# Optimization experiments

Measured on AMD Instinct MI355X. Metric: run time of the kernel, lower is better.

Reference implementation:

```python
import jax, jax.numpy as jnp
import numpy as np

B, N = 128, 196
ENC, DEC, ATT = 2048, 512, 512

def setup_inputs() -> dict:
    key = jax.random.key(0)
    ks = jax.random.split(key, 8)
    s_enc = 1.0 / np.sqrt(ENC)
    s_dec = 1.0 / np.sqrt(DEC)
    s_att = 1.0 / np.sqrt(ATT)
    return {
        "encoder_out": jax.random.normal(ks[0], (B, N, ENC), jnp.float32),
        "decoder_hidden": jax.random.normal(ks[1], (B, DEC), jnp.float32),
        "W_enc": jax.random.uniform(ks[2], (ENC, ATT), jnp.float32, -s_enc, s_enc),
        "b_enc": jax.random.uniform(ks[3], (ATT,), jnp.float32, -s_enc, s_enc),
        "W_dec": jax.random.uniform(ks[4], (DEC, ATT), jnp.float32, -s_dec, s_dec),
        "b_dec": jax.random.uniform(ks[5], (ATT,), jnp.float32, -s_dec, s_dec),
        "W_full": jax.random.uniform(ks[6], (ATT,), jnp.float32, -s_att, s_att),
        "b_full": jax.random.uniform(ks[7], (), jnp.float32, -s_att, s_att),
    }

def reference(encoder_out, decoder_hidden, W_enc, b_enc, W_dec, b_dec, W_full, b_full):
    # att1: [B, N, ATT]; att2: [B, 1, ATT]
    att1 = jnp.einsum('bne,ea->bna', encoder_out, W_enc) + b_enc
    att2 = decoder_hidden @ W_dec + b_dec
    combined = jax.nn.relu(att1 + att2[:, None, :])
    e = jnp.einsum('bna,a->bn', combined, W_full) + b_full  # [B, N]
    alpha = jax.nn.softmax(e, axis=1)
    attention_weighted_encoding = jnp.einsum('bne,bn->be', encoder_out, alpha)
    return attention_weighted_encoding, alpha
```

## Files before the change

### kernel.cpp

```cpp
#include <hip/hip_runtime.h>
#include <hip/hip_bf16.h>

#define BB   128
#define NN   196
#define MM   (BB*NN)
#define ENC  2048
#define ATT  512
#define DEC  512
#define BK   32
#define KSTEPS (ENC/BK)

using f32x4 = __attribute__((ext_vector_type(4))) float;
using s16x8 = __attribute__((ext_vector_type(8))) short;

__device__ __forceinline__ short f2bf(float f) {
    union { __hip_bfloat16 h; short s; } u;
    u.h = __float2bfloat16(f);
    return u.s;
}

__global__ void transpose_convert_kernel(const float* __restrict__ W,
                                         unsigned short* __restrict__ Wt) {
    __shared__ float tile[32][33];
    const int a0 = blockIdx.x * 32;
    const int k0 = blockIdx.y * 32;
    const int tx = threadIdx.x & 31, ty = threadIdx.x >> 5;
    #pragma unroll
    for (int i = 0; i < 32; i += 8)
        tile[ty + i][tx] = W[(size_t)(k0 + ty + i) * ATT + a0 + tx];
    __syncthreads();
    #pragma unroll
    for (int i = 0; i < 32; i += 8) {
        union { __hip_bfloat16 h; unsigned short u; } v;
        v.h = __float2bfloat16(tile[tx][ty + i]);
        Wt[(size_t)(a0 + ty + i) * ENC + k0 + tx] = v.u;
    }
}

__global__ void att2_kernel(const float* __restrict__ dec,
                            const float* __restrict__ Wd,
                            const float* __restrict__ bd,
                            const float* __restrict__ benc,
                            float* __restrict__ att2) {
    const int b  = blockIdx.x;
    const int c0 = blockIdx.y * 64;
    const int t  = threadIdx.x;
    const int cl = t & 63, kg = t >> 6;
    __shared__ float sdec[DEC];
    __shared__ float red[4][64];
    sdec[t]       = dec[b * DEC + t];
    sdec[t + 256] = dec[b * DEC + t + 256];
    __syncthreads();
    float acc = 0.f;
    const float* wp = Wd + c0 + cl;
    #pragma unroll 8
    for (int k = kg * 128; k < kg * 128 + 128; ++k)
        acc += sdec[k] * wp[(size_t)k * ATT];
    red[kg][cl] = acc;
    __syncthreads();
    if (t < 64) {
        float s = red[0][t] + red[1][t] + red[2][t] + red[3][t];
        att2[b * ATT + c0 + t] = s + bd[c0 + t] + benc[c0 + t];
    }
}

__global__ __launch_bounds__(256, 3)
void gemm_e_kernel(const float* __restrict__ enc,
                   const unsigned short* __restrict__ Wt,
                   const float* __restrict__ att2,
                   const float* __restrict__ Wf,
                   float* __restrict__ e_part) {
    __shared__ unsigned short sA[2][64 * 40];
    __shared__ unsigned short sB[2][256 * 32];
    __shared__ float e_sm[64];

    const int t    = threadIdx.x;
    const int lane = t & 63;
    const int w    = t >> 6;
    const int aBlk  = blockIdx.x;
    const int mBase = blockIdx.y * 64;
    const int aBase = aBlk * 256;
    const int r = lane & 15, q = lane >> 4;

    const int arow = t >> 2;
    const int akc  = (t & 3) * 8;
    const float* gA = enc + (size_t)(mBase + arow) * ENC + akc;
    const int wAoff = arow * 40 + akc;

    const unsigned short* gB[4];
    #pragma unroll
    for (int i = 0; i < 4; ++i) {
        int s = i * 256 + t;
        int brow = s >> 2;
        int ck = (s & 3) ^ ((brow >> 1) & 3);
        gB[i] = Wt + (size_t)(aBase + brow) * ENC + ck * 8;
    }

    int offA[4];
    #pragma unroll
    for (int mi = 0; mi < 4; ++mi)
        offA[mi] = (mi * 16 + r) * 40 + q * 8;
    int offB[4];
    #pragma unroll
    for (int ni = 0; ni < 4; ++ni) {
        int col = w * 64 + ni * 16 + r;
        offB[ni] = col * 32 + (q ^ ((col >> 1) & 3)) * 8;
    }

    f32x4 acc[4][4] = {};

    auto issueB = [&](int ks, int buf) {
        #pragma unroll
        for (int i = 0; i < 4; ++i)
            __builtin_amdgcn_global_load_lds(
                (const __attribute__((address_space(1))) void*)(gB[i] + (size_t)ks * BK),
                (__attribute__((address_space(3))) void*)(&sB[buf][0] + (i * 256 + w * 64) * 8),
                16, 0, 0);
    };
    auto storeA = [&](int buf, f32x4 x0, f32x4 x1) {
        s16x8 v;
        #pragma unroll
        for (int j = 0; j < 4; ++j) { v[j] = f2bf(x0[j]); v[4 + j] = f2bf(x1[j]); }
        *(s16x8*)(&sA[buf][0] + wAoff) = v;
    };
    auto compute = [&](int buf) {
        s16x8 af[4], bf[4];
        #pragma unroll
        for (int mi = 0; mi < 4; ++mi)
            af[mi] = *(const s16x8*)(&sA[buf][0] + offA[mi]);
        #pragma unroll
        for (int ni = 0; ni < 4; ++ni)
            bf[ni] = *(const s16x8*)(&sB[buf][0] + offB[ni]);
        #pragma unroll
        for (int mi = 0; mi < 4; ++mi)
            #pragma unroll
            for (int ni = 0; ni < 4; ++ni)
                acc[mi][ni] = __builtin_amdgcn_mfma_f32_16x16x32_bf16(
                    af[mi], bf[ni], acc[mi][ni], 0, 0, 0);
    };

    f32x4 a0, a1;
    {
        const float* p = gA;
        a0 = *(const f32x4*)p; a1 = *(const f32x4*)(p + 4);
    }
    issueB(0, 0);
    storeA(0, a0, a1);
    __syncthreads();

    #pragma unroll 1
    for (int ks = 1; ks < KSTEPS; ++ks) {
        const float* p = gA + (size_t)ks * BK;
        a0 = *(const f32x4*)p; a1 = *(const f32x4*)(p + 4);
        issueB(ks, ks & 1);
        compute((ks - 1) & 1);
        storeA(ks & 1, a0, a1);
        __syncthreads();
    }
    compute((KSTEPS - 1) & 1);

    if (t < 64) e_sm[t] = 0.f;
    __syncthreads();

    float wfv[4];
    #pragma unroll
    for (int ni = 0; ni < 4; ++ni)
        wfv[ni] = Wf[aBase + w * 64 + ni * 16 + r];

    #pragma unroll
    for (int mi = 0; mi < 4; ++mi) {
        #pragma unroll
        for (int reg = 0; reg < 4; ++reg) {
            int lrow = mi * 16 + q * 4 + reg;
            int gm = mBase + lrow;
            int b = gm / NN;
            const float* a2 = att2 + b * ATT + aBase + w * 64;
            float rs = 0.f;
            #pragma unroll
            for (int ni = 0; ni < 4; ++ni) {
                float v = acc[mi][ni][reg] + a2[ni * 16 + r];
                rs += fmaxf(v, 0.f) * wfv[ni];
            }
            atomicAdd(&e_sm[lrow], rs);
        }
    }
    __syncthreads();
    if (t < 64)
        e_part[(size_t)aBlk * MM + mBase + t] = e_sm[t];
}

__global__ void softmax_kernel(const float* __restrict__ e_part,
                               const float* __restrict__ b_full,
                               float* __restrict__ out,
                               float* __restrict__ alpha_ws) {
    const int b = blockIdx.x;
    const int t = threadIdx.x;
    __shared__ float sm[256];

    float v = -3.0e38f;
    if (t < NN) {
        int gm = b * NN + t;
        v = e_part[gm] + e_part[MM + gm] + b_full[0];
    }
    sm[t] = v;
    __syncthreads();
    for (int s = 128; s > 0; s >>= 1) {
        if (t < s) sm[t] = fmaxf(sm[t], sm[t + s]);
        __syncthreads();
    }
    float mx = sm[0];
    __syncthreads();
    float ex = (t < NN) ? __expf(v - mx) : 0.f;
    sm[t] = ex;
    __syncthreads();
    for (int s = 128; s > 0; s >>= 1) {
        if (t < s) sm[t] += sm[t + s];
        __syncthreads();
    }
    float inv = 1.0f / sm[0];
    if (t < NN) {
        float a = ex * inv;
        out[BB * ENC + b * NN + t] = a;
        alpha_ws[b * NN + t] = a;
    }
}

__global__ __launch_bounds__(64)
void awe_kernel(const float* __restrict__ enc,
                const float* __restrict__ alpha_ws,
                float* __restrict__ out) {
    const int b = blockIdx.x, chunk = blockIdx.y;
    const int l = threadIdx.x;
    __shared__ float al[NN];
    for (int n = l; n < NN; n += 64) al[n] = alpha_ws[b * NN + n];
    __syncthreads();

    const float* ep = enc + (size_t)b * NN * ENC + chunk * 256 + l * 4;
    f32x4 acc0 = {}, acc1 = {}, acc2 = {}, acc3 = {};
    #pragma unroll 2
    for (int n = 0; n < NN; n += 4) {
        f32x4 v0 = *(const f32x4*)(ep + (size_t)(n + 0) * ENC);
        f32x4 v1 = *(const f32x4*)(ep + (size_t)(n + 1) * ENC);
        f32x4 v2 = *(const f32x4*)(ep + (size_t)(n + 2) * ENC);
        f32x4 v3 = *(const f32x4*)(ep + (size_t)(n + 3) * ENC);
        acc0 += v0 * al[n];
        acc1 += v1 * al[n + 1];
        acc2 += v2 * al[n + 2];
        acc3 += v3 * al[n + 3];
    }
    f32x4 s = (acc0 + acc1) + (acc2 + acc3);
    *(f32x4*)(out + (size_t)b * ENC + chunk * 256 + l * 4) = s;
}

extern "C" void kernel_launch(void* const* d_in, const int* in_sizes, int n_in,
                              void* d_out, int out_size, void* d_ws, size_t ws_size,
                              hipStream_t stream) {
    const float* enc    = (const float*)d_in[0];
    const float* dec    = (const float*)d_in[1];
    const float* W_enc  = (const float*)d_in[2];
    const float* b_enc  = (const float*)d_in[3];
    const float* W_dec  = (const float*)d_in[4];
    const float* b_dec  = (const float*)d_in[5];
    const float* W_full = (const float*)d_in[6];
    const float* b_full = (const float*)d_in[7];
    float* out = (float*)d_out;

    char* ws = (char*)d_ws;
    unsigned short* Wt = (unsigned short*)ws;
    float* att2     = (float*)(ws + (size_t)ENC * ATT * 2);
    float* e_part   = (float*)(ws + (size_t)ENC * ATT * 2 + BB * ATT * 4);
    float* alpha_ws = (float*)(ws + (size_t)ENC * ATT * 2 + BB * ATT * 4
                               + (size_t)2 * MM * 4);

    transpose_convert_kernel<<<dim3(ATT / 32, ENC / 32), 256, 0, stream>>>(W_enc, Wt);
    att2_kernel<<<dim3(BB, 8), 256, 0, stream>>>(dec, W_dec, b_dec, b_enc, att2);
    gemm_e_kernel<<<dim3(2, MM / 64), 256, 0, stream>>>(enc, Wt, att2, W_full, e_part);
    softmax_kernel<<<BB, 256, 0, stream>>>(e_part, b_full, out, alpha_ws);
    awe_kernel<<<dim3(BB, 8), 64, 0, stream>>>(enc, alpha_ws, out);
}
```

Before: 472.9 us.

## Narrow GEMM tile to 128 columns, stream fp32 A via LDS, single-buffer

The GEMM kernel now uses 64x128 tiles instead of 64x256, and four column blocks write partial scores that the softmax sums. Encoder rows are copied as fp32 straight into swizzled LDS with direct global-to-LDS loads and converted to bf16 at fragment-read time, replacing the register-staged conversion. Double buffering is dropped for a single buffer with two barriers per step, and occupancy is raised to 5 waves. This halves the row reuse of A, so the fp32 encoder is read four times instead of twice. The e reduction now uses shuffles before the LDS atomic, and the awe kernel uses 256-thread blocks.

```diff
diff --git a/kernel.cpp b/kernel.cpp
--- a/kernel.cpp
+++ b/kernel.cpp
@@ -64,14 +64,14 @@
     }
 }
 
-__global__ __launch_bounds__(256, 3)
+__global__ __launch_bounds__(256, 5)
 void gemm_e_kernel(const float* __restrict__ enc,
                    const unsigned short* __restrict__ Wt,
                    const float* __restrict__ att2,
                    const float* __restrict__ Wf,
                    float* __restrict__ e_part) {
-    __shared__ unsigned short sA[2][64 * 40];
-    __shared__ unsigned short sB[2][256 * 32];
+    __shared__ float sA[64 * 32];
+    __shared__ unsigned short sB[128 * 32];
     __shared__ float e_sm[64];
 
     const int t    = threadIdx.x;
@@ -79,93 +79,88 @@
     const int w    = t >> 6;
     const int aBlk  = blockIdx.x;
     const int mBase = blockIdx.y * 64;
-    const int aBase = aBlk * 256;
+    const int aBase = aBlk * 128;
     const int r = lane & 15, q = lane >> 4;
 
-    const int arow = t >> 2;
-    const int akc  = (t & 3) * 8;
-    const float* gA = enc + (size_t)(mBase + arow) * ENC + akc;
-    const int wAoff = arow * 40 + akc;
-
-    const unsigned short* gB[4];
-    #pragma unroll
-    for (int i = 0; i < 4; ++i) {
+    const float* gA[2];
+    #pragma unroll
+    for (int i = 0; i < 2; ++i) {
         int s = i * 256 + t;
-        int brow = s >> 2;
-        int ck = (s & 3) ^ ((brow >> 1) & 3);
-        gB[i] = Wt + (size_t)(aBase + brow) * ENC + ck * 8;
-    }
-
-    int offA[4];
-    #pragma unroll
-    for (int mi = 0; mi < 4; ++mi)
-        offA[mi] = (mi * 16 + r) * 40 + q * 8;
-    int offB[4];
-    #pragma unroll
-    for (int ni = 0; ni < 4; ++ni) {
-        int col = w * 64 + ni * 16 + r;
-        offB[ni] = col * 32 + (q ^ ((col >> 1) & 3)) * 8;
-    }
-
-    f32x4 acc[4][4] = {};
-
-    auto issueB = [&](int ks, int buf) {
-        #pragma unroll
-        for (int i = 0; i < 4; ++i)
+        int row = s >> 3, ck = s & 7;
+        int g = ck ^ (row & 7);
+        gA[i] = enc + (size_t)(mBase + row) * ENC + g * 4;
+    }
+    const unsigned short* gB[2];
+    #pragma unroll
+    for (int i = 0; i < 2; ++i) {
+        int s = i * 256 + t;
+        int row = s >> 2, ck = s & 3;
+        int g = ck ^ ((row & 3) ^ ((row >> 2) & 3));
+        gB[i] = Wt + (size_t)(aBase + row) * ENC + g * 8;
+    }
+
+    int offA[4][2];
+    #pragma unroll
+    for (int mi = 0; mi < 4; ++mi) {
+        int row = mi * 16 + r;
+        offA[mi][0] = row * 128 + ((2 * q)     ^ (row & 7)) * 16;
+        offA[mi][1] = row * 128 + ((2 * q + 1) ^ (row & 7)) * 16;
+    }
+    int offB[2];
+    #pragma unroll
+    for (int ni = 0; ni < 2; ++ni) {
+        int col = w * 32 + ni * 16 + r;
+        offB[ni] = col * 64 + (q ^ ((col & 3) ^ ((col >> 2) & 3))) * 16;
+    }
+
+    f32x4 acc[4][2] = {};
+
+    #pragma unroll 1
+    for (int ks = 0; ks < KSTEPS; ++ks) {
+        #pragma unroll
+        for (int i = 0; i < 2; ++i)
+            __builtin_amdgcn_global_load_lds(
+                (const __attribute__((address_space(1))) void*)(gA[i] + (size_t)ks * BK),
+                (__attribute__((address_space(3))) void*)((char*)sA + (i * 256 + w * 64) * 16),
+                16, 0, 0);
+        #pragma unroll
+        for (int i = 0; i < 2; ++i)
             __builtin_amdgcn_global_load_lds(
                 (const __attribute__((address_space(1))) void*)(gB[i] + (size_t)ks * BK),
-                (__attribute__((address_space(3))) void*)(&sB[buf][0] + (i * 256 + w * 64) * 8),
+                (__attribute__((address_space(3))) void*)((char*)sB + (i * 256 + w * 64) * 16),
                 16, 0, 0);
-    };
-    auto storeA = [&](int buf, f32x4 x0, f32x4 x1) {
-        s16x8 v;
-        #pragma unroll
-        for (int j = 0; j < 4; ++j) { v[j] = f2bf(x0[j]); v[4 + j] = f2bf(x1[j]); }
-        *(s16x8*)(&sA[buf][0] + wAoff) = v;
-    };
-    auto compute = [&](int buf) {
-        s16x8 af[4], bf[4];
-        #pragma unroll
-        for (int mi = 0; mi < 4; ++mi)
-            af[mi] = *(const s16x8*)(&sA[buf][0] + offA[mi]);
-        #pragma unroll
-        for (int ni = 0; ni < 4; ++ni)
-            bf[ni] = *(const s16x8*)(&sB[buf][0] + offB[ni]);
+        __syncthreads();
+
+        s16x8 af[4], bf[2];
+        #pragma unroll
+        for (int mi = 0; mi < 4; ++mi) {
+            f32x4 f0 = *(const f32x4*)((const char*)sA + offA[mi][0]);
+            f32x4 f1 = *(const f32x4*)((const char*)sA + offA[mi][1]);
+            s16x8 a;
+            #pragma unroll
+            for (int j = 0; j < 4; ++j) { a[j] = f2bf(f0[j]); a[4 + j] = f2bf(f1[j]); }
+            af[mi] = a;
+        }
+        #pragma unroll
+        for (int ni = 0; ni < 2; ++ni)
+            bf[ni] = *(const s16x8*)((const char*)sB + offB[ni]);
+
         #pragma unroll
         for (int mi = 0; mi < 4; ++mi)
             #pragma unroll
-            for (int ni = 0; ni < 4; ++ni)
+            for (int ni = 0; ni < 2; ++ni)
                 acc[mi][ni] = __builtin_amdgcn_mfma_f32_16x16x32_bf16(
                     af[mi], bf[ni], acc[mi][ni], 0, 0, 0);
-    };
-
-    f32x4 a0, a1;
-    {
-        const float* p = gA;
-        a0 = *(const f32x4*)p; a1 = *(const f32x4*)(p + 4);
-    }
-    issueB(0, 0);
-    storeA(0, a0, a1);
-    __syncthreads();
-
-    #pragma unroll 1
-    for (int ks = 1; ks < KSTEPS; ++ks) {
-        const float* p = gA + (size_t)ks * BK;
-        a0 = *(const f32x4*)p; a1 = *(const f32x4*)(p + 4);
-        issueB(ks, ks & 1);
-        compute((ks - 1) & 1);
-        storeA(ks & 1, a0, a1);
-        __syncthreads();
-    }
-    compute((KSTEPS - 1) & 1);
+        __syncthreads();
+    }
 
     if (t < 64) e_sm[t] = 0.f;
     __syncthreads();
 
-    float wfv[4];
-    #pragma unroll
-    for (int ni = 0; ni < 4; ++ni)
-        wfv[ni] = Wf[aBase + w * 64 + ni * 16 + r];
+    float wfv[2];
+    #pragma unroll
+    for (int ni = 0; ni < 2; ++ni)
+        wfv[ni] = Wf[aBase + w * 32 + ni * 16 + r];
 
     #pragma unroll
     for (int mi = 0; mi < 4; ++mi) {
@@ -174,14 +169,18 @@
             int lrow = mi * 16 + q * 4 + reg;
             int gm = mBase + lrow;
             int b = gm / NN;
-            const float* a2 = att2 + b * ATT + aBase + w * 64;
+            const float* a2 = att2 + b * ATT + aBase + w * 32;
             float rs = 0.f;
             #pragma unroll
-            for (int ni = 0; ni < 4; ++ni) {
+            for (int ni = 0; ni < 2; ++ni) {
                 float v = acc[mi][ni][reg] + a2[ni * 16 + r];
                 rs += fmaxf(v, 0.f) * wfv[ni];
             }
-            atomicAdd(&e_sm[lrow], rs);
+            rs += __shfl_xor(rs, 1);
+            rs += __shfl_xor(rs, 2);
+            rs += __shfl_xor(rs, 4);
+            rs += __shfl_xor(rs, 8);
+            if (r == 0) atomicAdd(&e_sm[lrow], rs);
         }
     }
     __syncthreads();
@@ -200,7 +199,8 @@
     float v = -3.0e38f;
     if (t < NN) {
         int gm = b * NN + t;
-        v = e_part[gm] + e_part[MM + gm] + b_full[0];
+        v = e_part[gm] + e_part[MM + gm] + e_part[2 * MM + gm] + e_part[3 * MM + gm]
+            + b_full[0];
     }
     sm[t] = v;
     __syncthreads();
@@ -225,17 +225,17 @@
     }
 }
 
-__global__ __launch_bounds__(64)
+__global__ __launch_bounds__(256)
 void awe_kernel(const float* __restrict__ enc,
                 const float* __restrict__ alpha_ws,
                 float* __restrict__ out) {
     const int b = blockIdx.x, chunk = blockIdx.y;
-    const int l = threadIdx.x;
+    const int t = threadIdx.x;
     __shared__ float al[NN];
-    for (int n = l; n < NN; n += 64) al[n] = alpha_ws[b * NN + n];
-    __syncthreads();
-
-    const float* ep = enc + (size_t)b * NN * ENC + chunk * 256 + l * 4;
+    if (t < NN) al[t] = alpha_ws[b * NN + t];
+    __syncthreads();
+
+    const float* ep = enc + (size_t)b * NN * ENC + chunk * 1024 + t * 4;
     f32x4 acc0 = {}, acc1 = {}, acc2 = {}, acc3 = {};
     #pragma unroll 2
     for (int n = 0; n < NN; n += 4) {
@@ -249,7 +249,7 @@
         acc3 += v3 * al[n + 3];
     }
     f32x4 s = (acc0 + acc1) + (acc2 + acc3);
-    *(f32x4*)(out + (size_t)b * ENC + chunk * 256 + l * 4) = s;
+    *(f32x4*)(out + (size_t)b * ENC + chunk * 1024 + t * 4) = s;
 }
 
 extern "C" void kernel_launch(void* const* d_in, const int* in_sizes, int n_in,
@@ -270,11 +270,11 @@
     float* att2     = (float*)(ws + (size_t)ENC * ATT * 2);
     float* e_part   = (float*)(ws + (size_t)ENC * ATT * 2 + BB * ATT * 4);
     float* alpha_ws = (float*)(ws + (size_t)ENC * ATT * 2 + BB * ATT * 4
-                               + (size_t)2 * MM * 4);
+                               + (size_t)4 * MM * 4);
 
     transpose_convert_kernel<<<dim3(ATT / 32, ENC / 32), 256, 0, stream>>>(W_enc, Wt);
     att2_kernel<<<dim3(BB, 8), 256, 0, stream>>>(dec, W_dec, b_dec, b_enc, att2);
-    gemm_e_kernel<<<dim3(2, MM / 64), 256, 0, stream>>>(enc, Wt, att2, W_full, e_part);
+    gemm_e_kernel<<<dim3(4, MM / 64), 256, 0, stream>>>(enc, Wt, att2, W_full, e_part);
     softmax_kernel<<<BB, 256, 0, stream>>>(e_part, b_full, out, alpha_ws);
-    awe_kernel<<<dim3(BB, 8), 64, 0, stream>>>(enc, alpha_ws, out);
-}
+    awe_kernel<<<dim3(BB, 2), 256, 0, stream>>>(enc, alpha_ws, out);
+}
```

After: 457.2 us. 3.3% less time.
